# Performance work log

Measured on AMD Instinct MI355X. Metric: run time of the kernel, lower is better.

Reference implementation:

```python
import jax, jax.numpy as jnp
import numpy as np

B, N, K = 128, 512, 6      # graphs, nodes per graph, kNN neighbors
IN_FEAT, POS_DIM, H = 128, 3, 256
NB = B * N                  # total nodes
EPS_BN = 1e-5


def setup_inputs() -> dict:
    key = jax.random.key(0)
    ks = jax.random.split(key, 32)
    inp = {
        "x": jax.random.normal(ks[0], (NB, IN_FEAT), dtype=jnp.float32),
        "pos": jax.random.normal(ks[1], (NB, POS_DIM), dtype=jnp.float32) * 5.0,
    }
    d_in = IN_FEAT + POS_DIM
    def lin(k, fi, fo):
        s = 1.0 / np.sqrt(fi)
        return jax.random.uniform(k, (fi, fo), jnp.float32, -s, s)
    # GCN layers
    inp["W1"] = lin(ks[2], d_in, H); inp["b1"] = jnp.zeros((H,), jnp.float32)
    inp["W2"] = lin(ks[3], H, H);    inp["b2"] = jnp.zeros((H,), jnp.float32)
    inp["W3"] = lin(ks[4], H, H);    inp["b3"] = jnp.zeros((H,), jnp.float32)
    # BatchNorm (eval mode: running stats)
    for i, km, kv in [(1, ks[5], ks[6]), (2, ks[7], ks[8]), (3, ks[9], ks[10])]:
        inp[f"g{i}"]  = jnp.ones((H,), jnp.float32)
        inp[f"be{i}"] = jnp.zeros((H,), jnp.float32)
        inp[f"m{i}"]  = jax.random.normal(km, (H,), jnp.float32) * 0.1
        inp[f"v{i}"]  = jax.random.uniform(kv, (H,), jnp.float32, 0.5, 1.5)
    # attention gate, heads
    inp["gate_w"] = lin(ks[11], H, 1); inp["gate_b"] = jnp.zeros((1,), jnp.float32)
    inp["aff_w"]  = lin(ks[12], H, 1); inp["aff_b"]  = jnp.zeros((1,), jnp.float32)
    inp["rl_w1"]  = lin(ks[13], H, H); inp["rl_b1"]  = jnp.zeros((H,), jnp.float32)
    inp["rl_w2"]  = lin(ks[14], H, POS_DIM); inp["rl_b2"] = jnp.zeros((POS_DIM,), jnp.float32)
    return inp


def _knn_edges(pos):
    # torch_geometric knn_graph semantics: per-graph k nearest neighbors,
    # no self loops, edges (neighbor -> node).  batch = repeat(arange(B), N).
    p = pos.reshape(B, N, POS_DIM)
    sq = jnp.sum(p * p, axis=-1)                                  # [B,N]
    d2 = sq[:, :, None] + sq[:, None, :] - 2.0 * jnp.einsum("bnd,bmd->bnm", p, p)
    d2 = jnp.where(jnp.eye(N, dtype=bool)[None], jnp.inf, d2)     # exclude self
    _, idx = jax.lax.top_k(-d2, K)                                # [B,N,K] local nbr ids
    offs = (jnp.arange(B) * N)[:, None, None]
    src = (idx + offs).reshape(-1)                                # neighbor (source)
    dst = jnp.repeat(jnp.arange(NB), K)                           # target node
    return src, dst


def _gcn(h, W, b, src, dst):
    # GCNConv: add self loops, symmetric norm D^-1/2 (A+I) D^-1/2
    hw = h @ W                                                    # [NB,H]
    deg = jax.ops.segment_sum(jnp.ones_like(dst, jnp.float32), dst, num_segments=NB) + 1.0
    dis = jax.lax.rsqrt(deg)
    norm = dis[src] * dis[dst]                                    # [E]
    agg = jax.ops.segment_sum(hw[src] * norm[:, None], dst, num_segments=NB)
    agg = agg + hw * (1.0 / deg)[:, None]                          # self loop term
    return agg + b


def _bn(h, g, be, m, v):
    return (h - m) * (g * jax.lax.rsqrt(v + EPS_BN)) + be


def reference(x, pos, W1, b1, W2, b2, W3, b3,
              g1, be1, m1, v1, g2, be2, m2, v2, g3, be3, m3, v3,
              gate_w, gate_b, aff_w, aff_b, rl_w1, rl_b1, rl_w2, rl_b2):
    src, dst = _knn_edges(pos)
    h = jnp.concatenate([x, pos], axis=1)                          # [NB, in_feat+3]
    h = jax.nn.relu(_bn(_gcn(h, W1, b1, src, dst), g1, be1, m1, v1))
    h = jax.nn.relu(_bn(_gcn(h, W2, b2, src, dst), g2, be2, m2, v2))
    h = jax.nn.relu(_bn(_gcn(h, W3, b3, src, dst), g3, be3, m3, v3))
    # (dropout is identity in eval mode)
    gate = jax.nn.relu(h @ gate_w + gate_b)[:, 0]                  # [NB]
    attn = jax.nn.softmax(gate.reshape(B, N), axis=1)              # scatter_softmax over batch
    gemb = jnp.einsum("bn,bnh->bh", attn, h.reshape(B, N, H))      # scatter_add of weighted x
    affinity = gemb @ aff_w + aff_b                                # [B,1]
    pose = jax.nn.relu(gemb @ rl_w1 + rl_b1) @ rl_w2 + rl_b2        # [B,3]
    return affinity, pose
```

## Files before the change

### kernel.cpp

```cpp
#include <hip/hip_runtime.h>
#include <hip/hip_bf16.h>
#include <math.h>
#include <float.h>

#define NBG 128
#define NND 512
#define KNN 6
#define NB_TOT (NBG*NND)
#define HF 256
#define NSTEP1 5

typedef short bf16x8 __attribute__((ext_vector_type(8)));
typedef float f32x4 __attribute__((ext_vector_type(4)));

__device__ __forceinline__ int swzoff(int row, int kbyte) {
    return (row*64 + kbyte) ^ (((row>>1)&3)<<4);
}

__device__ __forceinline__ void split_store(const float* v, char* hi_p, char* lo_p) {
    bf16x8 hi, lo;
    #pragma unroll
    for (int j = 0; j < 8; ++j) {
        __hip_bfloat16 h = __float2bfloat16(v[j]);
        float hf = __bfloat162float(h);
        __hip_bfloat16 l = __float2bfloat16(v[j] - hf);
        hi[j] = *(short*)&h;
        lo[j] = *(short*)&l;
    }
    *(bf16x8*)hi_p = hi;
    *(bf16x8*)lo_p = lo;
}

__device__ __forceinline__ int xcd_swz(int bid, int grid) {
    return (bid & 7) * (grid >> 3) + (bid >> 3);
}

__global__ __launch_bounds__(256) void knn_kernel(const float* __restrict__ pos,
                                                  unsigned short* __restrict__ nbr)
{
    const int blk = blockIdx.x;
    const int g = blk >> 3;
    const int chunk = (blk & 7) * 64;
    const int tid = threadIdx.x;
    const int node = chunk + (tid >> 2);
    const int sub = tid & 3;

    __shared__ float4 p4[NND + (NND>>6)];
    const float* pg = pos + (size_t)g * NND * 3;
    for (int n = tid; n < NND; n += 256) {
        float x = pg[n*3+0], y = pg[n*3+1], z = pg[n*3+2];
        p4[n + (n>>6)] = make_float4(x, y, z, x*x + y*y + z*z);
    }
    __syncthreads();

    const float4 pi = p4[node + (node>>6)];
    const float m2x = -2.0f*pi.x, m2y = -2.0f*pi.y, m2z = -2.0f*pi.z;

    float bdA[KNN], bdB[KNN]; int biA[KNN], biB[KNN];
    #pragma unroll
    for (int q = 0; q < KNN; ++q) {
        bdA[q] = FLT_MAX; biA[q] = 0x7fffffff;
        bdB[q] = FLT_MAX; biB[q] = 0x7fffffff;
    }

    const int j0 = sub * 128;
    const float4* baseA = &p4[sub*130];
    const float4* baseB = &p4[sub*130 + 65];

    #pragma unroll 2
    for (int t = 0; t < 64; ++t) {
        int ja = j0 + t, jb = j0 + 64 + t;
        float4 pa = baseA[t];
        float4 pb = baseB[t];
        float da = fmaf(m2z, pa.z, fmaf(m2y, pa.y, fmaf(m2x, pa.x, pa.w)));
        float db = fmaf(m2z, pb.z, fmaf(m2y, pb.y, fmaf(m2x, pb.x, pb.w)));
        da = (ja == node) ? FLT_MAX : da;
        db = (jb == node) ? FLT_MAX : db;
        float ca = da; int ia = ja;
        float cb = db; int ib = jb;
        #pragma unroll
        for (int q = 0; q < KNN; ++q) {
            bool sa = ca < bdA[q];
            float t1 = sa ? ca : bdA[q]; float t2 = sa ? bdA[q] : ca;
            int   t3 = sa ? ia : biA[q]; int   t4 = sa ? biA[q] : ia;
            bdA[q] = t1; ca = t2; biA[q] = t3; ia = t4;
            bool sb = cb < bdB[q];
            float u1 = sb ? cb : bdB[q]; float u2 = sb ? bdB[q] : cb;
            int   u3 = sb ? ib : biB[q]; int   u4 = sb ? biB[q] : ib;
            bdB[q] = u1; cb = u2; biB[q] = u3; ib = u4;
        }
    }

    float ld[KNN]; int li[KNN];
    #pragma unroll
    for (int q = 0; q < KNN; ++q) {
        float ad = bdA[q], xd = bdB[KNN-1-q];
        int   ai = biA[q], xi = biB[KNN-1-q];
        bool t = (ad < xd) || (ad == xd && ai < xi);
        ld[q] = t ? ad : xd;
        li[q] = t ? ai : xi;
    }
    #pragma unroll
    for (int pass = 0; pass < KNN-1; ++pass)
        #pragma unroll
        for (int a = 0; a < KNN-1-pass; ++a) {
            int b = a+1;
            bool sw = (ld[b] < ld[a]) || (ld[b] == ld[a] && li[b] < li[a]);
            float td = sw ? ld[b] : ld[a]; float ud = sw ? ld[a] : ld[b];
            int   ti = sw ? li[b] : li[a]; int   ui = sw ? li[a] : li[b];
            ld[a] = td; li[a] = ti; ld[b] = ud; li[b] = ui;
        }

    #pragma unroll
    for (int mi = 0; mi < 2; ++mi) {
        const int mask = 1 << mi;
        float od[KNN]; int oi[KNN];
        #pragma unroll
        for (int q = 0; q < KNN; ++q) {
            od[q] = __shfl_xor(ld[q], mask);
            oi[q] = __shfl_xor(li[q], mask);
        }
        #pragma unroll
        for (int q = 0; q < KNN; ++q) {
            float ad = ld[q], xd = od[KNN-1-q];
            int   ai = li[q], xi = oi[KNN-1-q];
            bool t = (ad < xd) || (ad == xd && ai < xi);
            ld[q] = t ? ad : xd;
            li[q] = t ? ai : xi;
        }
        #pragma unroll
        for (int pass = 0; pass < KNN-1; ++pass)
            #pragma unroll
            for (int a = 0; a < KNN-1-pass; ++a) {
                int b = a+1;
                bool sw = (ld[b] < ld[a]) || (ld[b] == ld[a] && li[b] < li[a]);
                float td = sw ? ld[b] : ld[a]; float ud = sw ? ld[a] : ld[b];
                int   ti = sw ? li[b] : li[a]; int   ui = sw ? li[a] : li[b];
                ld[a] = td; li[a] = ti; ld[b] = ud; li[b] = ui;
            }
    }

    if (sub == 0) {
        int base = (g*NND + node)*KNN;
        #pragma unroll
        for (int q = 0; q < KNN; ++q) nbr[base+q] = (unsigned short)li[q];
    }
}

__global__ __launch_bounds__(256) void prew_all(
    const float* __restrict__ W1, const float* __restrict__ W2,
    const float* __restrict__ W3,
    char* __restrict__ I1, char* __restrict__ I2, char* __restrict__ I3)
{
    int b = blockIdx.x;
    const float* W; char* img; int K, nstep;
    if (b < 20)      { W = W1; img = I1; K = 131; nstep = 5; }
    else if (b < 52) { W = W2; img = I2; K = 256; nstep = 8; b -= 20; }
    else             { W = W3; img = I3; K = 256; nstep = 8; b -= 52; }
    int gid = b*256 + threadIdx.x;
    int per_nb = nstep*512;
    int nb = gid / per_nb;
    int r  = gid - nb*per_nb;
    int step = r >> 9;
    int r2 = r & 511;
    int cl = r2 >> 2;
    int kc = (r2 & 3) * 8;
    float v[8];
    #pragma unroll
    for (int j = 0; j < 8; ++j) {
        int gk = step*32 + kc + j;
        v[j] = (gk < K) ? W[(size_t)gk*256 + nb*128 + cl] : 0.f;
    }
    char* base = img + (size_t)nb*nstep*16384 + (size_t)step*16384;
    int off = swzoff(cl, kc*2);
    split_store(v, base + off, base + 8192 + off);
}

__global__ __launch_bounds__(256) void agg_first(const float* __restrict__ x,
                                                 const float* __restrict__ pos,
                                                 const unsigned short* __restrict__ nbr,
                                                 char* __restrict__ Aimg)
{
    int gid = xcd_swz(blockIdx.x, gridDim.x)*256 + threadIdx.x;
    int i = gid / 20, ch = gid - i*20;
    const float rs = 1.0f/sqrtf(7.0f);
    const float c1 = rs*rs, c2 = 1.0f/7.0f;
    const int gbase = i & ~(NND-1);
    float v[8];
    if (ch < 16) {
        int jn[KNN];
        #pragma unroll
        for (int q = 0; q < KNN; ++q) jn[q] = gbase + nbr[i*KNN+q];
        const float4* x4 = (const float4*)x;
        int c4 = ch*2;
        float4 s0 = x4[(size_t)i*32 + c4], s1 = x4[(size_t)i*32 + c4 + 1];
        float a0=0,a1=0,a2=0,a3=0,b0=0,b1=0,b2=0,b3=0;
        #pragma unroll
        for (int q = 0; q < KNN; ++q) {
            float4 t0 = x4[(size_t)jn[q]*32 + c4];
            float4 t1 = x4[(size_t)jn[q]*32 + c4 + 1];
            a0+=t0.x; a1+=t0.y; a2+=t0.z; a3+=t0.w;
            b0+=t1.x; b1+=t1.y; b2+=t1.z; b3+=t1.w;
        }
        v[0]=a0*c1+s0.x*c2; v[1]=a1*c1+s0.y*c2; v[2]=a2*c1+s0.z*c2; v[3]=a3*c1+s0.w*c2;
        v[4]=b0*c1+s1.x*c2; v[5]=b1*c1+s1.y*c2; v[6]=b2*c1+s1.z*c2; v[7]=b3*c1+s1.w*c2;
    } else if (ch == 16) {
        int jn[KNN];
        #pragma unroll
        for (int q = 0; q < KNN; ++q) jn[q] = gbase + nbr[i*KNN+q];
        float ax=0, ay=0, az=0;
        #pragma unroll
        for (int q = 0; q < KNN; ++q) {
            ax += pos[(size_t)jn[q]*3+0];
            ay += pos[(size_t)jn[q]*3+1];
            az += pos[(size_t)jn[q]*3+2];
        }
        v[0] = ax*c1 + pos[(size_t)i*3+0]*c2;
        v[1] = ay*c1 + pos[(size_t)i*3+1]*c2;
        v[2] = az*c1 + pos[(size_t)i*3+2]*c2;
        v[3]=v[4]=v[5]=v[6]=v[7]=0.f;
    } else {
        #pragma unroll
        for (int j = 0; j < 8; ++j) v[j] = 0.f;
    }
    int mb = i >> 7, row = i & 127, step = ch >> 2, kbyte = (ch & 3)*16;
    char* base = Aimg + (size_t)mb*(NSTEP1*16384) + (size_t)step*16384;
    int off = swzoff(row, kbyte);
    split_store(v, base + off, base + 8192 + off);
}

__global__ __launch_bounds__(256,4) void gemm_mfma(
    const char* __restrict__ Aimg, const char* __restrict__ Wimg, int nstep,
    const float* __restrict__ bias,
    const float* __restrict__ gam, const float* __restrict__ bet,
    const float* __restrict__ mu,  const float* __restrict__ var,
    float* __restrict__ out)
{
    __shared__ uint4 lds4[34816/16];
    char* lds  = (char*)lds4;
    char* Alds = lds;
    char* Wlds = lds + 16384;
    float* scs = (float*)(lds + 32768);
    float* shs = scs + 256;
    const int tid = threadIdx.x;
    const int lane = tid & 63, wave = tid >> 6;
    const int wm = wave >> 1, wn = wave & 1;
    const int mblk = blockIdx.x, nblk = blockIdx.y;

    if (tid < 256) {
        float s = gam[tid] / sqrtf(var[tid] + 1e-5f);
        scs[tid] = s;
        shs[tid] = bet[tid] + (bias[tid] - mu[tid]) * s;
    }

    const char* Ab = Aimg + (size_t)mblk * nstep * 16384;
    const char* Wb = Wimg + (size_t)nblk * nstep * 16384;

    const char* gbase; char* lbase;
    int soff;
    if (wave < 2) { gbase = Ab;  lbase = Alds; soff = wave*8192; }
    else          { gbase = Wb;  lbase = Wlds; soff = (wave-2)*8192; }

    f32x4 acc[4][4];
    #pragma unroll
    for (int m = 0; m < 4; ++m)
        #pragma unroll
        for (int n = 0; n < 4; ++n) acc[m][n] = (f32x4){0.f,0.f,0.f,0.f};

    for (int s = 0; s < nstep; ++s) {
        #pragma unroll
        for (int i = 0; i < 8; ++i) {
            int off = soff + i*1024;
            __builtin_amdgcn_global_load_lds(
                (const __attribute__((address_space(1))) void*)(gbase + (size_t)s*16384 + off + lane*16),
                (__attribute__((address_space(3))) void*)(lbase + off), 16, 0, 0);
        }
        __syncthreads();
        const int kb = (lane >> 4) * 16;
        bf16x8 ah[4], al[4];
        #pragma unroll
        for (int m = 0; m < 4; ++m) {
            int row = wm*64 + m*16 + (lane & 15);
            int off = swzoff(row, kb);
            ah[m] = *(const bf16x8*)(Alds + off);
            al[m] = *(const bf16x8*)(Alds + 8192 + off);
        }
        #pragma unroll
        for (int n = 0; n < 4; ++n) {
            int col = wn*64 + n*16 + (lane & 15);
            int off = swzoff(col, kb);
            bf16x8 bh = *(const bf16x8*)(Wlds + off);
            bf16x8 bl = *(const bf16x8*)(Wlds + 8192 + off);
            #pragma unroll
            for (int m = 0; m < 4; ++m) {
                acc[m][n] = __builtin_amdgcn_mfma_f32_16x16x32_bf16(ah[m], bh, acc[m][n], 0, 0, 0);
                acc[m][n] = __builtin_amdgcn_mfma_f32_16x16x32_bf16(al[m], bh, acc[m][n], 0, 0, 0);
                acc[m][n] = __builtin_amdgcn_mfma_f32_16x16x32_bf16(ah[m], bl, acc[m][n], 0, 0, 0);
            }
        }
        __syncthreads();
    }

    #pragma unroll
    for (int n = 0; n < 4; ++n) {
        int c = nblk*128 + wn*64 + n*16 + (lane & 15);
        float sc = scs[c], sh = shs[c];
        #pragma unroll
        for (int m = 0; m < 4; ++m) {
            int r0 = mblk*128 + wm*64 + m*16 + (lane >> 4)*4;
            #pragma unroll
            for (int q = 0; q < 4; ++q) {
                float v = acc[m][n][q]*sc + sh;
                out[(size_t)(r0+q)*256 + c] = fmaxf(v, 0.f);
            }
        }
    }
}

__global__ __launch_bounds__(256,3) void gcn_fused(
    const float* __restrict__ hin,
    const unsigned short* __restrict__ nbr,
    const char* __restrict__ Wimg,
    const float* __restrict__ bias,
    const float* __restrict__ gam, const float* __restrict__ bet,
    const float* __restrict__ mu,  const float* __restrict__ var,
    float* __restrict__ hout,
    const float* __restrict__ gate_w, float* __restrict__ gatep)
{
    __shared__ uint4 lds4[44032/16];
    char* Alds = (char*)lds4;
    char* Wlds = (char*)lds4 + 8192;
    float* scs = (float*)((char*)lds4 + 40960);
    float* shs = scs + 256;
    float* gred = (float*)((char*)lds4 + 43008);
    const int tid = threadIdx.x;
    const int lane = tid & 63, wave = tid >> 6;
    const int wn = wave;
    const int mblk = xcd_swz(blockIdx.x, gridDim.x);

    {
        float s = gam[tid] / sqrtf(var[tid] + 1e-5f);
        scs[tid] = s;
        shs[tid] = bet[tid] + (bias[tid] - mu[tid]) * s;
    }

    const int arow = tid >> 2, ch = tid & 3;
    const int gnode = mblk*64 + arow;
    const int gb = gnode & ~(NND-1);
    int jn[KNN];
    #pragma unroll
    for (int q = 0; q < KNN; ++q) jn[q] = gb + nbr[gnode*KNN + q];
    const float rs = 1.0f/sqrtf(7.0f);
    const float c1 = rs*rs, c2 = 1.0f/7.0f;
    const int aoff = swzoff(arow, ch*16);
    const float4* h4 = (const float4*)hin;

    f32x4 acc[4][4];
    #pragma unroll
    for (int m = 0; m < 4; ++m)
        #pragma unroll
        for (int n = 0; n < 4; ++n) acc[m][n] = (f32x4){0.f,0.f,0.f,0.f};

    float4 pf[14];
    {
        const int fb = ch*2;
        #pragma unroll
        for (int q = 0; q < KNN; ++q) {
            pf[2*q]   = h4[(size_t)jn[q]*64 + fb];
            pf[2*q+1] = h4[(size_t)jn[q]*64 + fb + 1];
        }
        pf[12] = h4[(size_t)gnode*64 + fb];
        pf[13] = h4[(size_t)gnode*64 + fb + 1];
    }

    for (int s = 0; s < 8; ++s) {
        {
            float a0 = pf[0].x + pf[2].x + pf[4].x + pf[6].x + pf[8].x + pf[10].x;
            float a1 = pf[0].y + pf[2].y + pf[4].y + pf[6].y + pf[8].y + pf[10].y;
            float a2 = pf[0].z + pf[2].z + pf[4].z + pf[6].z + pf[8].z + pf[10].z;
            float a3 = pf[0].w + pf[2].w + pf[4].w + pf[6].w + pf[8].w + pf[10].w;
            float b0 = pf[1].x + pf[3].x + pf[5].x + pf[7].x + pf[9].x + pf[11].x;
            float b1 = pf[1].y + pf[3].y + pf[5].y + pf[7].y + pf[9].y + pf[11].y;
            float b2 = pf[1].z + pf[3].z + pf[5].z + pf[7].z + pf[9].z + pf[11].z;
            float b3 = pf[1].w + pf[3].w + pf[5].w + pf[7].w + pf[9].w + pf[11].w;
            float v[8];
            v[0]=a0*c1+pf[12].x*c2; v[1]=a1*c1+pf[12].y*c2;
            v[2]=a2*c1+pf[12].z*c2; v[3]=a3*c1+pf[12].w*c2;
            v[4]=b0*c1+pf[13].x*c2; v[5]=b1*c1+pf[13].y*c2;
            v[6]=b2*c1+pf[13].z*c2; v[7]=b3*c1+pf[13].w*c2;
            split_store(v, Alds + aoff, Alds + 4096 + aoff);
        }
        #pragma unroll
        for (int i = 0; i < 8; ++i) {
            int woff = i*4096 + wave*1024;
            size_t srcoff = (woff < 16384) ? ((size_t)s*16384 + woff)
                                           : ((size_t)(8+s)*16384 + (woff - 16384));
            __builtin_amdgcn_global_load_lds(
                (const __attribute__((address_space(1))) void*)(Wimg + srcoff + lane*16),
                (__attribute__((address_space(3))) void*)(Wlds + woff), 16, 0, 0);
        }
        __syncthreads();
        if (s < 7) {
            const int fb = (s+1)*8 + ch*2;
            #pragma unroll
            for (int q = 0; q < KNN; ++q) {
                pf[2*q]   = h4[(size_t)jn[q]*64 + fb];
                pf[2*q+1] = h4[(size_t)jn[q]*64 + fb + 1];
            }
            pf[12] = h4[(size_t)gnode*64 + fb];
            pf[13] = h4[(size_t)gnode*64 + fb + 1];
        }
        const int kb = (lane >> 4) * 16;
        bf16x8 ah[4], al[4];
        #pragma unroll
        for (int m = 0; m < 4; ++m) {
            int o = swzoff(m*16 + (lane & 15), kb);
            ah[m] = *(const bf16x8*)(Alds + o);
            al[m] = *(const bf16x8*)(Alds + 4096 + o);
        }
        const char* wreg = Wlds + (wn >> 1)*16384;
        #pragma unroll
        for (int n = 0; n < 4; ++n) {
            int cl = (wn & 1)*64 + n*16 + (lane & 15);
            int o = swzoff(cl, kb);
            bf16x8 bh = *(const bf16x8*)(wreg + o);
            bf16x8 bl = *(const bf16x8*)(wreg + 8192 + o);
            #pragma unroll
            for (int m = 0; m < 4; ++m) {
                acc[m][n] = __builtin_amdgcn_mfma_f32_16x16x32_bf16(ah[m], bh, acc[m][n], 0, 0, 0);
                acc[m][n] = __builtin_amdgcn_mfma_f32_16x16x32_bf16(al[m], bh, acc[m][n], 0, 0, 0);
                acc[m][n] = __builtin_amdgcn_mfma_f32_16x16x32_bf16(ah[m], bl, acc[m][n], 0, 0, 0);
            }
        }
        __syncthreads();
    }

    const bool dogate = (gatep != nullptr);
    float gp[4][4];
    #pragma unroll
    for (int m = 0; m < 4; ++m)
        #pragma unroll
        for (int q = 0; q < 4; ++q) gp[m][q] = 0.f;

    #pragma unroll
    for (int n = 0; n < 4; ++n) {
        int c = wn*64 + n*16 + (lane & 15);
        float sc = scs[c], sh = shs[c];
        float gwv = dogate ? gate_w[c] : 0.f;
        #pragma unroll
        for (int m = 0; m < 4; ++m) {
            int r0 = mblk*64 + m*16 + (lane >> 4)*4;
            #pragma unroll
            for (int q = 0; q < 4; ++q) {
                float v = fmaxf(acc[m][n][q]*sc + sh, 0.f);
                hout[(size_t)(r0+q)*256 + c] = v;
                gp[m][q] = fmaf(v, gwv, gp[m][q]);
            }
        }
    }

    if (dogate) {
        #pragma unroll
        for (int m = 0; m < 4; ++m)
            #pragma unroll
            for (int q = 0; q < 4; ++q) {
                float s = gp[m][q];
                s += __shfl_xor(s, 1); s += __shfl_xor(s, 2);
                s += __shfl_xor(s, 4); s += __shfl_xor(s, 8);
                gp[m][q] = s;
            }
        if ((lane & 15) == 0) {
            #pragma unroll
            for (int m = 0; m < 4; ++m)
                #pragma unroll
                for (int q = 0; q < 4; ++q)
                    gred[wn*64 + m*16 + (lane >> 4)*4 + q] = gp[m][q];
        }
        __syncthreads();
        if (tid < 64)
            gatep[mblk*64 + tid] = (gred[tid] + gred[64 + tid])
                                 + (gred[128 + tid] + gred[192 + tid]);
    }
}

__device__ __forceinline__ float blk_sum256(float v, volatile float* red)
{
    #pragma unroll
    for (int o = 32; o > 0; o >>= 1) v += __shfl_xor(v, o, 64);
    __syncthreads();
    if ((threadIdx.x & 63) == 0) red[threadIdx.x >> 6] = v;
    __syncthreads();
    return (red[0] + red[1]) + (red[2] + red[3]);
}

__global__ __launch_bounds__(256) void gemb_kernel(const float* __restrict__ h3,
                                                   const float* __restrict__ gatep,
                                                   const float* __restrict__ gate_b,
                                                   float* __restrict__ gembp)
{
    const int g = blockIdx.x, s = blockIdx.y;
    const int tid = threadIdx.x, lane = tid & 63, w = tid >> 6;
    __shared__ float at[128];
    __shared__ float red4[4][HF];
    __shared__ float red[4];

    float gb = gate_b[0];
    float g0 = fmaxf(gatep[g*NND + tid] + gb, 0.f);
    float g1 = fmaxf(gatep[g*NND + 256 + tid] + gb, 0.f);
    float m = fmaxf(g0, g1);
    #pragma unroll
    for (int o = 32; o > 0; o >>= 1) m = fmaxf(m, __shfl_xor(m, o, 64));
    if ((tid & 63) == 0) red[tid >> 6] = m;
    __syncthreads();
    m = fmaxf(fmaxf(red[0], red[1]), fmaxf(red[2], red[3]));
    float S = blk_sum256(expf(g0 - m) + expf(g1 - m), red);
    if (tid < 128) {
        float gv = fmaxf(gatep[g*NND + s*128 + tid] + gb, 0.f);
        at[tid] = expf(gv - m) / S;
    }
    __syncthreads();

    const float* hb = h3 + (size_t)(g*NND + s*128 + w*32) * HF;
    float4 acc = make_float4(0.f, 0.f, 0.f, 0.f);
    #pragma unroll 4
    for (int n = 0; n < 32; ++n) {
        float a = at[w*32 + n];
        float4 v = ((const float4*)(hb + (size_t)n*HF))[lane];
        acc.x = fmaf(a, v.x, acc.x); acc.y = fmaf(a, v.y, acc.y);
        acc.z = fmaf(a, v.z, acc.z); acc.w = fmaf(a, v.w, acc.w);
    }
    *(float4*)&red4[w][lane*4] = acc;
    __syncthreads();
    if (tid < HF) {
        float sum = (red4[0][tid] + red4[1][tid]) + (red4[2][tid] + red4[3][tid]);
        gembp[((size_t)s*NBG + g)*HF + tid] = sum;
    }
}

__global__ __launch_bounds__(256) void heads_kernel(
    const float* __restrict__ gembp,
    const float* __restrict__ aff_w,  const float* __restrict__ aff_b,
    const float* __restrict__ rl_w1,  const float* __restrict__ rl_b1,
    const float* __restrict__ rl_w2,  const float* __restrict__ rl_b2,
    float* __restrict__ out)
{
    int g = blockIdx.x, tid = threadIdx.x;
    __shared__ float gemb[HF];
    __shared__ float red[4];
    float acc = (gembp[((size_t)0*NBG + g)*HF + tid] + gembp[((size_t)1*NBG + g)*HF + tid])
              + (gembp[((size_t)2*NBG + g)*HF + tid] + gembp[((size_t)3*NBG + g)*HF + tid]);
    gemb[tid] = acc;
    __syncthreads();

    float sa = blk_sum256(acc * aff_w[tid], red);
    if (tid == 0) out[g] = sa + aff_b[0];

    float t = rl_b1[tid];
    #pragma unroll 4
    for (int k2 = 0; k2 < HF; ++k2)
        t = fmaf(gemb[k2], rl_w1[(size_t)k2*HF + tid], t);
    t = fmaxf(t, 0.f);
    float s0 = blk_sum256(t * rl_w2[(size_t)tid*3 + 0], red);
    if (tid == 0) out[128 + g*3 + 0] = s0 + rl_b2[0];
    float s1 = blk_sum256(t * rl_w2[(size_t)tid*3 + 1], red);
    if (tid == 0) out[128 + g*3 + 1] = s1 + rl_b2[1];
    float s2 = blk_sum256(t * rl_w2[(size_t)tid*3 + 2], red);
    if (tid == 0) out[128 + g*3 + 2] = s2 + rl_b2[2];
}

extern "C" void kernel_launch(void* const* d_in, const int* in_sizes, int n_in,
                              void* d_out, int out_size, void* d_ws, size_t ws_size,
                              hipStream_t stream)
{
    const float* x      = (const float*)d_in[0];
    const float* pos    = (const float*)d_in[1];
    const float* W1     = (const float*)d_in[2];
    const float* b1     = (const float*)d_in[3];
    const float* W2     = (const float*)d_in[4];
    const float* b2     = (const float*)d_in[5];
    const float* W3     = (const float*)d_in[6];
    const float* b3     = (const float*)d_in[7];
    const float* g1     = (const float*)d_in[8];
    const float* be1    = (const float*)d_in[9];
    const float* m1     = (const float*)d_in[10];
    const float* v1     = (const float*)d_in[11];
    const float* g2     = (const float*)d_in[12];
    const float* be2    = (const float*)d_in[13];
    const float* m2     = (const float*)d_in[14];
    const float* v2     = (const float*)d_in[15];
    const float* g3     = (const float*)d_in[16];
    const float* be3    = (const float*)d_in[17];
    const float* m3     = (const float*)d_in[18];
    const float* v3     = (const float*)d_in[19];
    const float* gate_w = (const float*)d_in[20];
    const float* gate_b = (const float*)d_in[21];
    const float* aff_w  = (const float*)d_in[22];
    const float* aff_b  = (const float*)d_in[23];
    const float* rl_w1  = (const float*)d_in[24];
    const float* rl_b1  = (const float*)d_in[25];
    const float* rl_w2  = (const float*)d_in[26];
    const float* rl_b2  = (const float*)d_in[27];
    float* out = (float*)d_out;

    char* wsb = (char*)d_ws;
    unsigned short* nbr = (unsigned short*)wsb;
    char* Wimg1 = wsb + 786432;
    char* Wimg2 = Wimg1 + (size_t)2*NSTEP1*16384;
    char* Wimg3 = Wimg2 + (size_t)2*8*16384;
    float* h_a  = (float*)(Wimg3 + (size_t)2*8*16384);
    char* regB  = (char*)(h_a + (size_t)NB_TOT*HF);
    float* gatep = (float*)Wimg1;
    char*  Aimg  = regB;
    float* h_b   = (float*)regB;
    float* gembp = (float*)regB;

    knn_kernel<<<NBG*8, 256, 0, stream>>>(pos, nbr);
    prew_all<<<84, 256, 0, stream>>>(W1, W2, W3, Wimg1, Wimg2, Wimg3);

    agg_first<<<(NB_TOT*20)/256, 256, 0, stream>>>(x, pos, nbr, Aimg);
    gemm_mfma<<<dim3(NB_TOT/128, 2), 256, 0, stream>>>(Aimg, Wimg1, NSTEP1,
        b1, g1, be1, m1, v1, h_a);
    gcn_fused<<<NB_TOT/64, 256, 0, stream>>>(h_a, nbr, Wimg2,
        b2, g2, be2, m2, v2, h_b, gate_w, nullptr);
    gcn_fused<<<NB_TOT/64, 256, 0, stream>>>(h_b, nbr, Wimg3,
        b3, g3, be3, m3, v3, h_a, gate_w, gatep);

    gemb_kernel<<<dim3(NBG, 4), 256, 0, stream>>>(h_a, gatep, gate_b, gembp);
    heads_kernel<<<NBG, 256, 0, stream>>>(gembp, aff_w, aff_b,
                                          rl_w1, rl_b1, rl_w2, rl_b2, out);
}
```

Measured before the change: 211.3 us.

## Split fused GCN layer over two column halves per node block

Each 64-node block of the fused gather+GEMM kernel is now split across two workgroups, each computing 128 output columns. Per-block LDS and accumulator registers are halved, so the launch bound goes from 3 to 4 blocks per CU and the grid doubles. The cost is that every half redoes the neighbour gather and aggregation, which doubles the gather traffic. Because of that, the gate partial sums are now combined with atomics into a buffer cleared by an extra memset, and that buffer is relocated to Wimg2, which is no longer read at that point.

Result: slower. 230.9 us (+9.3%).

```diff
diff --git a/kernel.cpp b/kernel.cpp
--- a/kernel.cpp
+++ b/kernel.cpp
@@ -317,7 +317,7 @@
     }
 }
 
-__global__ __launch_bounds__(256,3) void gcn_fused(
+__global__ __launch_bounds__(256,4) void gcn_fused(
     const float* __restrict__ hin,
     const unsigned short* __restrict__ nbr,
     const char* __restrict__ Wimg,
@@ -327,16 +327,17 @@
     float* __restrict__ hout,
     const float* __restrict__ gate_w, float* __restrict__ gatep)
 {
-    __shared__ uint4 lds4[44032/16];
+    __shared__ uint4 lds4[27648/16];
     char* Alds = (char*)lds4;
     char* Wlds = (char*)lds4 + 8192;
-    float* scs = (float*)((char*)lds4 + 40960);
+    float* scs = (float*)((char*)lds4 + 24576);
     float* shs = scs + 256;
-    float* gred = (float*)((char*)lds4 + 43008);
+    float* gred = (float*)((char*)lds4 + 26624);
     const int tid = threadIdx.x;
     const int lane = tid & 63, wave = tid >> 6;
     const int wn = wave;
-    const int mblk = xcd_swz(blockIdx.x, gridDim.x);
+    const int bid = xcd_swz(blockIdx.x, gridDim.x);
+    const int nb = bid & 1, mblk = bid >> 1;
 
     {
         float s = gam[tid] / sqrtf(var[tid] + 1e-5f);
@@ -354,12 +355,13 @@
     const float c1 = rs*rs, c2 = 1.0f/7.0f;
     const int aoff = swzoff(arow, ch*16);
     const float4* h4 = (const float4*)hin;
-
-    f32x4 acc[4][4];
+    const char* wbase = Wimg + (size_t)nb * 8 * 16384;
+
+    f32x4 acc[4][2];
     #pragma unroll
     for (int m = 0; m < 4; ++m)
         #pragma unroll
-        for (int n = 0; n < 4; ++n) acc[m][n] = (f32x4){0.f,0.f,0.f,0.f};
+        for (int n = 0; n < 2; ++n) acc[m][n] = (f32x4){0.f,0.f,0.f,0.f};
 
     float4 pf[14];
     {
@@ -391,12 +393,10 @@
             split_store(v, Alds + aoff, Alds + 4096 + aoff);
         }
         #pragma unroll
-        for (int i = 0; i < 8; ++i) {
+        for (int i = 0; i < 4; ++i) {
             int woff = i*4096 + wave*1024;
-            size_t srcoff = (woff < 16384) ? ((size_t)s*16384 + woff)
-                                           : ((size_t)(8+s)*16384 + (woff - 16384));
             __builtin_amdgcn_global_load_lds(
-                (const __attribute__((address_space(1))) void*)(Wimg + srcoff + lane*16),
+                (const __attribute__((address_space(1))) void*)(wbase + (size_t)s*16384 + woff + lane*16),
                 (__attribute__((address_space(3))) void*)(Wlds + woff), 16, 0, 0);
         }
         __syncthreads();
@@ -418,13 +418,12 @@
             ah[m] = *(const bf16x8*)(Alds + o);
             al[m] = *(const bf16x8*)(Alds + 4096 + o);
         }
-        const char* wreg = Wlds + (wn >> 1)*16384;
-        #pragma unroll
-        for (int n = 0; n < 4; ++n) {
-            int cl = (wn & 1)*64 + n*16 + (lane & 15);
+        #pragma unroll
+        for (int n = 0; n < 2; ++n) {
+            int cl = wn*32 + n*16 + (lane & 15);
             int o = swzoff(cl, kb);
-            bf16x8 bh = *(const bf16x8*)(wreg + o);
-            bf16x8 bl = *(const bf16x8*)(wreg + 8192 + o);
+            bf16x8 bh = *(const bf16x8*)(Wlds + o);
+            bf16x8 bl = *(const bf16x8*)(Wlds + 8192 + o);
             #pragma unroll
             for (int m = 0; m < 4; ++m) {
                 acc[m][n] = __builtin_amdgcn_mfma_f32_16x16x32_bf16(ah[m], bh, acc[m][n], 0, 0, 0);
@@ -443,8 +442,8 @@
         for (int q = 0; q < 4; ++q) gp[m][q] = 0.f;
 
     #pragma unroll
-    for (int n = 0; n < 4; ++n) {
-        int c = wn*64 + n*16 + (lane & 15);
+    for (int n = 0; n < 2; ++n) {
+        int c = nb*128 + wn*32 + n*16 + (lane & 15);
         float sc = scs[c], sh = shs[c];
         float gwv = dogate ? gate_w[c] : 0.f;
         #pragma unroll
@@ -477,9 +476,11 @@
                     gred[wn*64 + m*16 + (lane >> 4)*4 + q] = gp[m][q];
         }
         __syncthreads();
-        if (tid < 64)
-            gatep[mblk*64 + tid] = (gred[tid] + gred[64 + tid])
-                                 + (gred[128 + tid] + gred[192 + tid]);
+        if (tid < 64) {
+            float v = (gred[tid] + gred[64 + tid])
+                    + (gred[128 + tid] + gred[192 + tid]);
+            atomicAdd(&gatep[mblk*64 + tid], v);
+        }
     }
 }
 
@@ -609,7 +610,7 @@
     char* Wimg3 = Wimg2 + (size_t)2*8*16384;
     float* h_a  = (float*)(Wimg3 + (size_t)2*8*16384);
     char* regB  = (char*)(h_a + (size_t)NB_TOT*HF);
-    float* gatep = (float*)Wimg1;
+    float* gatep = (float*)Wimg2;
     char*  Aimg  = regB;
     float* h_b   = (float*)regB;
     float* gembp = (float*)regB;
@@ -620,9 +621,10 @@
     agg_first<<<(NB_TOT*20)/256, 256, 0, stream>>>(x, pos, nbr, Aimg);
     gemm_mfma<<<dim3(NB_TOT/128, 2), 256, 0, stream>>>(Aimg, Wimg1, NSTEP1,
         b1, g1, be1, m1, v1, h_a);
-    gcn_fused<<<NB_TOT/64, 256, 0, stream>>>(h_a, nbr, Wimg2,
+    gcn_fused<<<(NB_TOT/64)*2, 256, 0, stream>>>(h_a, nbr, Wimg2,
         b2, g2, be2, m2, v2, h_b, gate_w, nullptr);
-    gcn_fused<<<NB_TOT/64, 256, 0, stream>>>(h_b, nbr, Wimg3,
+    hipMemsetAsync(gatep, 0, (size_t)NB_TOT*4, stream);
+    gcn_fused<<<(NB_TOT/64)*2, 256, 0, stream>>>(h_b, nbr, Wimg3,
         b3, g3, be3, m3, v3, h_a, gate_w, gatep);
 
     gemb_kernel<<<dim3(NBG, 4), 256, 0, stream>>>(h_a, gatep, gate_b, gembp);
```
